# Kernel optimization log

Hardware: AMD Instinct MI355X
Metric: run time of the kernel (lower is better)

Reference implementation:

```python
import jax, jax.numpy as jnp
import numpy as np

B, T, E, H = 4, 1024, 1024, 16
F = E // H  # head_feature = 64
EPS = 1e-5


def setup_inputs() -> dict:
    key = jax.random.key(0)
    ks = jax.random.split(key, 7)
    return {
        "x": jax.random.normal(ks[0], (B, T, E), dtype=jnp.float32),
        "q_w": jax.random.normal(ks[1], (H, E, F), dtype=jnp.float32),
        "k_w": jax.random.normal(ks[2], (H, E, F), dtype=jnp.float32),
        "v_w": jax.random.normal(ks[3], (H, E, F), dtype=jnp.float32),
        "fr_w": jax.random.normal(ks[4], (B, E, E), dtype=jnp.float32),
        "ff_w": jax.random.normal(ks[5], (E, E), dtype=jnp.float32),
        "ff_b": jax.random.normal(ks[6], (E,), dtype=jnp.float32),
        "ln1_w": jnp.ones((T, E), dtype=jnp.float32),
        "ln1_b": jnp.zeros((T, E), dtype=jnp.float32),
        "ln2_w": jnp.ones((T, E), dtype=jnp.float32),
        "ln2_b": jnp.zeros((T, E), dtype=jnp.float32),
    }


def _layernorm_2d(x, w, b):
    # LayerNorm over the last TWO dims ([T, E]), matching nn.LayerNorm([T, E])
    mean = jnp.mean(x, axis=(-2, -1), keepdims=True)
    var = jnp.mean(jnp.square(x - mean), axis=(-2, -1), keepdims=True)
    return (x - mean) * jax.lax.rsqrt(var + EPS) * w + b


def _attention(x, q_w, k_w, v_w, fr_w):
    # projections: [B,T,E] x [H,E,F] -> [B,H,T,F]
    q = jnp.einsum("bte,hef->bhtf", x, q_w)
    k = jnp.einsum("bte,hef->bhtf", x, k_w)
    v = jnp.einsum("bte,hef->bhtf", x, v_w)
    scores = jnp.einsum("bhqf,bhkf->bhqk", q, k)  # [B,H,T,T]
    # faithful to source: multiplicative mask (-1e9 on strict upper tri, +1 added everywhere)
    ones = jnp.ones((T, T), dtype=scores.dtype)
    mask = -1.0e9 * jnp.triu(ones, k=1) + ones
    scores = scores * mask
    attn = jax.nn.softmax(scores / jnp.sqrt(jnp.float32(F)), axis=-1)
    z = jnp.einsum("bhqk,bhkf->bhqf", attn, v)  # [B,H,T,F]
    z = z.transpose(0, 2, 1, 3).reshape(B, T, E)  # merge heads
    return jnp.einsum("bte,bed->btd", z, fr_w)  # per-batch feature reduction


def reference(x, q_w, k_w, v_w, fr_w, ff_w, ff_b, ln1_w, ln1_b, ln2_w, ln2_b):
    z = _attention(x, q_w, k_w, v_w, fr_w)
    z1 = _layernorm_2d(x + z, ln1_w, ln1_b)
    z2 = jax.nn.relu(jnp.einsum("bte,de->btd", z1, ff_w) + ff_b)
    return _layernorm_2d(z1 + z2, ln2_w, ln2_b)
```

## Files before the change

### kernel.cpp

```cpp
#include <hip/hip_runtime.h>
#include <math.h>

constexpr int Bc = 4, Tc = 1024, Ec = 1024, Hc = 16, Fc = 64;

typedef __attribute__((ext_vector_type(8))) short bf16x8;
typedef __attribute__((ext_vector_type(4))) float f32x4;

__device__ __forceinline__ ushort f2bf(float x) {
  union { float f; unsigned u; } v; v.f = x;
  unsigned r = v.u + 0x7fffu + ((v.u >> 16) & 1u);
  return (ushort)(r >> 16);
}
__device__ __forceinline__ float bf2f(ushort h) {
  union { float f; unsigned u; } v; v.u = ((unsigned)h) << 16; return v.f;
}
__device__ __forceinline__ void split3(float x, ushort& h, ushort& m, ushort& l) {
  h = f2bf(x);
  float r1 = x - bf2f(h);
  m = f2bf(r1);
  float r2 = r1 - bf2f(m);
  l = f2bf(r2);
}
__device__ __forceinline__ void split2(float x, ushort& h, ushort& l) {
  h = f2bf(x);
  l = f2bf(x - bf2f(h));
}
__device__ __forceinline__ void split3t(float x, ushort& h, ushort& m, ushort& l) {
  union { float f; unsigned u; } v; v.f = x;
  h = (ushort)(v.u >> 16);
  union { float f; unsigned u; } hf; hf.u = v.u & 0xffff0000u;
  float r1 = x - hf.f;
  union { float f; unsigned u; } v1; v1.f = r1;
  m = (ushort)(v1.u >> 16);
  union { float f; unsigned u; } mf; mf.u = v1.u & 0xffff0000u;
  float r2 = r1 - mf.f;
  union { float f; unsigned u; } v2; v2.f = r2;
  l = (ushort)(v2.u >> 16);
}

#define FRAG_IDX(tile, quad, l) (((((tile) * 4) + (quad)) * 16 + (l)) * 8)

__global__ __launch_bounds__(256) void transp_w(
    const float* __restrict__ qw, const float* __restrict__ kw,
    const float* __restrict__ vw, ushort* __restrict__ wT)
{
  const int zi = blockIdx.z;
  const float* src = (zi == 0) ? qw : (zi == 1) ? kw : vw;
  ushort* dst = wT + (size_t)(zi * 3) * (1u << 20);
  const int ns = (zi == 2) ? 1 : 3;
  const int h = blockIdx.y, e0 = blockIdx.x * 64;
  __shared__ float T[64][68];
  const int tid = threadIdx.x;
  {
    const int er = tid >> 4, fr = (tid & 15) * 4;
#pragma unroll
    for (int i = 0; i < 4; ++i) {
      const float4 v = *(const float4*)&src[((size_t)(h * 1024 + e0 + er + i * 16)) * 64 + fr];
      *(float4*)&T[er + i * 16][fr] = v;
    }
  }
  __syncthreads();
  const int f = tid >> 2, eo = (tid & 3) * 16;
  ushort hs[16], ms[16], ls[16];
#pragma unroll
  for (int j = 0; j < 16; ++j) split3(T[eo + j][f], hs[j], ms[j], ls[j]);
  const size_t nbase = (size_t)(h * 64 + f) * 1024 + e0 + eo;
  bf16x8 v0, v1;
#pragma unroll
  for (int j = 0; j < 8; ++j) { v0[j] = (short)hs[j]; v1[j] = (short)hs[j + 8]; }
  *(bf16x8*)&dst[nbase] = v0; *(bf16x8*)&dst[nbase + 8] = v1;
  if (ns == 3) {
#pragma unroll
    for (int j = 0; j < 8; ++j) { v0[j] = (short)ms[j]; v1[j] = (short)ms[j + 8]; }
    *(bf16x8*)&dst[(1u << 20) + nbase] = v0; *(bf16x8*)&dst[(1u << 20) + nbase + 8] = v1;
#pragma unroll
    for (int j = 0; j < 8; ++j) { v0[j] = (short)ls[j]; v1[j] = (short)ls[j + 8]; }
    *(bf16x8*)&dst[(2u << 20) + nbase] = v0; *(bf16x8*)&dst[(2u << 20) + nbase + 8] = v1;
  }
}

__global__ __launch_bounds__(256) void transp_frw(
    const float* __restrict__ frw, ushort* __restrict__ frT)
{
  const int bb = blockIdx.z;
  const int e0 = blockIdx.x * 64, d0 = blockIdx.y * 64;
  __shared__ float T[64][68];
  const int tid = threadIdx.x;
  {
    const int er = tid >> 4, dr = (tid & 15) * 4;
#pragma unroll
    for (int i = 0; i < 4; ++i) {
      const float4 v = *(const float4*)&frw[((size_t)bb * 1024 + e0 + er + i * 16) * 1024 + d0 + dr];
      *(float4*)&T[er + i * 16][dr] = v;
    }
  }
  __syncthreads();
  const int d = tid >> 2, eo = (tid & 3) * 16;
  ushort hs[16], ls[16];
#pragma unroll
  for (int j = 0; j < 16; ++j) split2(T[eo + j][d], hs[j], ls[j]);
  const size_t nbase = ((size_t)bb * 1024 + d0 + d) * 1024 + e0 + eo;
  bf16x8 v0, v1;
#pragma unroll
  for (int j = 0; j < 8; ++j) { v0[j] = (short)hs[j]; v1[j] = (short)hs[j + 8]; }
  *(bf16x8*)&frT[nbase] = v0; *(bf16x8*)&frT[nbase + 8] = v1;
#pragma unroll
  for (int j = 0; j < 8; ++j) { v0[j] = (short)ls[j]; v1[j] = (short)ls[j + 8]; }
  *(bf16x8*)&frT[(4u << 20) + nbase] = v0; *(bf16x8*)&frT[(4u << 20) + nbase + 8] = v1;
}

__global__ __launch_bounds__(256) void proj_all_mfma(
    const float* __restrict__ x, const ushort* __restrict__ wT,
    float* __restrict__ qf, ushort* __restrict__ kh,
    ushort* __restrict__ km, ushort* __restrict__ kl,
    ushort* __restrict__ vt)
{
  const int zi = blockIdx.z;
  const int m0 = blockIdx.x * 128, n0 = blockIdx.y * 128;
  __shared__ ushort As[3 * 4096];
  __shared__ ushort Bs[3 * 4096];
  const int tid = threadIdx.x;
  const int wave = tid >> 6, lane = tid & 63, l15 = lane & 15, quad = lane >> 4;
  const int wm = wave >> 1, wn = wave & 1;
  const int sr = tid >> 1, q0 = (tid & 1) * 2;
  const int wb0 = FRAG_IDX(sr >> 4, q0, sr & 15);
  const int wb1 = FRAG_IDX(sr >> 4, q0 + 1, sr & 15);
  f32x4 acc[4][4] = {};

  if (zi < 2) {
    const ushort* wt = wT + (size_t)zi * 3 * (1u << 20);
    for (int k0 = 0; k0 < 1024; k0 += 32) {
      __syncthreads();
      {
        const float* ap = x + (size_t)(m0 + sr) * 1024 + k0 + q0 * 8;
        float xs[16];
        *(float4*)&xs[0]  = *(const float4*)(ap);
        *(float4*)&xs[4]  = *(const float4*)(ap + 4);
        *(float4*)&xs[8]  = *(const float4*)(ap + 8);
        *(float4*)&xs[12] = *(const float4*)(ap + 12);
        bf16x8 h0, h1, m0v, m1v, l0, l1;
#pragma unroll
        for (int j = 0; j < 8; ++j) {
          ushort hu, mu, lu;
          split3t(xs[j], hu, mu, lu);
          h0[j] = (short)hu; m0v[j] = (short)mu; l0[j] = (short)lu;
          split3t(xs[j + 8], hu, mu, lu);
          h1[j] = (short)hu; m1v[j] = (short)mu; l1[j] = (short)lu;
        }
        *(bf16x8*)&As[wb0] = h0;          *(bf16x8*)&As[wb1] = h1;
        *(bf16x8*)&As[4096 + wb0] = m0v;  *(bf16x8*)&As[4096 + wb1] = m1v;
        *(bf16x8*)&As[8192 + wb0] = l0;   *(bf16x8*)&As[8192 + wb1] = l1;
#pragma unroll
        for (int s = 0; s < 3; ++s) {
          const ushort* bp = wt + ((size_t)s << 20) + (size_t)(n0 + sr) * 1024 + k0 + q0 * 8;
          *(bf16x8*)&Bs[s * 4096 + wb0] = *(const bf16x8*)(bp);
          *(bf16x8*)&Bs[s * 4096 + wb1] = *(const bf16x8*)(bp + 8);
        }
      }
      __syncthreads();
      bf16x8 af[4][3];
#pragma unroll
      for (int tm = 0; tm < 4; ++tm)
#pragma unroll
        for (int s = 0; s < 3; ++s)
          af[tm][s] = *(const bf16x8*)&As[s * 4096 + FRAG_IDX(wm * 4 + tm, quad, l15)];
#pragma unroll
      for (int tn = 0; tn < 4; ++tn) {
        const int bi = FRAG_IDX(wn * 4 + tn, quad, l15);
        bf16x8 b0 = *(const bf16x8*)&Bs[bi];
        bf16x8 b1 = *(const bf16x8*)&Bs[4096 + bi];
        bf16x8 b2 = *(const bf16x8*)&Bs[8192 + bi];
#pragma unroll
        for (int tm = 0; tm < 4; ++tm) {
          f32x4 a = acc[tm][tn];
          a = __builtin_amdgcn_mfma_f32_16x16x32_bf16(af[tm][0], b0, a, 0, 0, 0);
          a = __builtin_amdgcn_mfma_f32_16x16x32_bf16(af[tm][0], b1, a, 0, 0, 0);
          a = __builtin_amdgcn_mfma_f32_16x16x32_bf16(af[tm][1], b0, a, 0, 0, 0);
          a = __builtin_amdgcn_mfma_f32_16x16x32_bf16(af[tm][0], b2, a, 0, 0, 0);
          a = __builtin_amdgcn_mfma_f32_16x16x32_bf16(af[tm][1], b1, a, 0, 0, 0);
          a = __builtin_amdgcn_mfma_f32_16x16x32_bf16(af[tm][2], b0, a, 0, 0, 0);
          acc[tm][tn] = a;
        }
      }
    }
#pragma unroll
    for (int tm = 0; tm < 4; ++tm) {
#pragma unroll
      for (int tn = 0; tn < 4; ++tn) {
#pragma unroll
        for (int r = 0; r < 4; ++r) {
          int m = m0 + wm * 64 + tm * 16 + quad * 4 + r;
          int n = n0 + wn * 64 + tn * 16 + l15;
          int b = m >> 10, t = m & 1023, h = n >> 6, f = n & 63;
          size_t idx = (((size_t)(b * 16 + h)) * 1024 + t) * 64 + f;
          if (zi == 0) {
            qf[idx] = acc[tm][tn][r];
          } else {
            ushort hu, mu, lu;
            split3(acc[tm][tn][r], hu, mu, lu);
            kh[idx] = hu; km[idx] = mu; kl[idx] = lu;
          }
        }
      }
    }
  } else {
    const ushort* wt = wT + (size_t)6 * (1u << 20);
    for (int k0 = 0; k0 < 1024; k0 += 32) {
      __syncthreads();
      {
        const float* ap = x + (size_t)(m0 + sr) * 1024 + k0 + q0 * 8;
        float xs[16];
        *(float4*)&xs[0]  = *(const float4*)(ap);
        *(float4*)&xs[4]  = *(const float4*)(ap + 4);
        *(float4*)&xs[8]  = *(const float4*)(ap + 8);
        *(float4*)&xs[12] = *(const float4*)(ap + 12);
        bf16x8 h0, h1;
#pragma unroll
        for (int j = 0; j < 8; ++j) {
          h0[j] = (short)f2bf(xs[j]);
          h1[j] = (short)f2bf(xs[j + 8]);
        }
        *(bf16x8*)&As[wb0] = h0; *(bf16x8*)&As[wb1] = h1;
        const ushort* bp = wt + (size_t)(n0 + sr) * 1024 + k0 + q0 * 8;
        *(bf16x8*)&Bs[wb0] = *(const bf16x8*)(bp);
        *(bf16x8*)&Bs[wb1] = *(const bf16x8*)(bp + 8);
      }
      __syncthreads();
      bf16x8 af[4];
#pragma unroll
      for (int tm = 0; tm < 4; ++tm)
        af[tm] = *(const bf16x8*)&As[FRAG_IDX(wm * 4 + tm, quad, l15)];
#pragma unroll
      for (int tn = 0; tn < 4; ++tn) {
        bf16x8 b0 = *(const bf16x8*)&Bs[FRAG_IDX(wn * 4 + tn, quad, l15)];
#pragma unroll
        for (int tm = 0; tm < 4; ++tm)
          acc[tm][tn] = __builtin_amdgcn_mfma_f32_16x16x32_bf16(af[tm], b0, acc[tm][tn], 0, 0, 0);
      }
    }
#pragma unroll
    for (int tm = 0; tm < 4; ++tm) {
#pragma unroll
      for (int tn = 0; tn < 4; ++tn) {
#pragma unroll
        for (int r = 0; r < 4; ++r) {
          int m = m0 + wm * 64 + tm * 16 + quad * 4 + r;
          int n = n0 + wn * 64 + tn * 16 + l15;
          int b = m >> 10, t = m & 1023, h = n >> 6, f = n & 63;
          vt[(((size_t)(b * 16 + h)) * 64 + f) * 1024 + t] = f2bf(acc[tm][tn][r]);
        }
      }
    }
  }
}

__global__ __launch_bounds__(512) void attn_mfma(
    const float* __restrict__ qf, const ushort* __restrict__ kh,
    const ushort* __restrict__ km, const ushort* __restrict__ kl,
    const ushort* __restrict__ vt, ushort* __restrict__ zh, ushort* __restrict__ zl)
{
  __shared__ ushort Ks[3][64][68];
  __shared__ ushort Vs[64][68];
  __shared__ ushort Pl[8][16][68];

  const int tid = threadIdx.x;
  const int wave = tid >> 6, lane = tid & 63;
  const int l15 = lane & 15, quad = lane >> 4;
  const int bh = blockIdx.y;
  const int qbase = blockIdx.x * 128;

  bf16x8 aqh[2], aqm[2], aql[2];
  {
    const int qrow = qbase + wave * 16 + l15;
    const float* qp = qf + ((size_t)bh * Tc + qrow) * Fc;
#pragma unroll
    for (int ks = 0; ks < 2; ++ks) {
      int f0 = ks * 32 + quad * 8;
      float4 x0 = *(const float4*)(qp + f0);
      float4 x1 = *(const float4*)(qp + f0 + 4);
      float xs[8] = {x0.x, x0.y, x0.z, x0.w, x1.x, x1.y, x1.z, x1.w};
#pragma unroll
      for (int j = 0; j < 8; ++j) {
        ushort hu, mu, lu;
        split3(xs[j], hu, mu, lu);
        aqh[ks][j] = (short)hu; aqm[ks][j] = (short)mu; aql[ks][j] = (short)lu;
      }
    }
  }

  f32x4 o[4] = {{0,0,0,0},{0,0,0,0},{0,0,0,0},{0,0,0,0}};
  float m_run[4], l_run[4];
#pragma unroll
  for (int r = 0; r < 4; ++r) { m_run[r] = -1e30f; l_run[r] = 0.f; }

  const int srow = tid >> 3, sc8 = tid & 7;
  const size_t kbase = (size_t)bh * Tc * Fc;
  const size_t vbase = (size_t)bh * Fc * Tc;
  const ushort* kp0 = kh + kbase + (size_t)srow * Fc + sc8 * 8;
  const ushort* kp1 = km + kbase + (size_t)srow * Fc + sc8 * 8;
  const ushort* kp2 = kl + kbase + (size_t)srow * Fc + sc8 * 8;
  const ushort* vp  = vt + vbase + (size_t)srow * Tc + sc8 * 8;

  for (int kt = 0; kt < Tc; kt += 64) {
    __syncthreads();
    {
      const size_t ko = (size_t)kt * Fc;
      *(bf16x8*)&Ks[0][srow][sc8 * 8] = *(const bf16x8*)(kp0 + ko);
      *(bf16x8*)&Ks[1][srow][sc8 * 8] = *(const bf16x8*)(kp1 + ko);
      *(bf16x8*)&Ks[2][srow][sc8 * 8] = *(const bf16x8*)(kp2 + ko);
      *(bf16x8*)&Vs[srow][sc8 * 8]    = *(const bf16x8*)(vp + kt);
    }
    __syncthreads();

    f32x4 sacc[4] = {{0,0,0,0},{0,0,0,0},{0,0,0,0},{0,0,0,0}};
#pragma unroll
    for (int nt = 0; nt < 4; ++nt) {
      int key = nt * 16 + l15;
#pragma unroll
      for (int ks = 0; ks < 2; ++ks) {
        int f0 = ks * 32 + quad * 8;
        bf16x8 bh_ = *(const bf16x8*)&Ks[0][key][f0];
        bf16x8 bm_ = *(const bf16x8*)&Ks[1][key][f0];
        bf16x8 bl_ = *(const bf16x8*)&Ks[2][key][f0];
        sacc[nt] = __builtin_amdgcn_mfma_f32_16x16x32_bf16(aqh[ks], bh_, sacc[nt], 0, 0, 0);
        sacc[nt] = __builtin_amdgcn_mfma_f32_16x16x32_bf16(aqh[ks], bm_, sacc[nt], 0, 0, 0);
        sacc[nt] = __builtin_amdgcn_mfma_f32_16x16x32_bf16(aqm[ks], bh_, sacc[nt], 0, 0, 0);
        sacc[nt] = __builtin_amdgcn_mfma_f32_16x16x32_bf16(aqh[ks], bl_, sacc[nt], 0, 0, 0);
        sacc[nt] = __builtin_amdgcn_mfma_f32_16x16x32_bf16(aqm[ks], bm_, sacc[nt], 0, 0, 0);
        sacc[nt] = __builtin_amdgcn_mfma_f32_16x16x32_bf16(aql[ks], bh_, sacc[nt], 0, 0, 0);
      }
    }

    const int rowg0 = qbase + wave * 16 + quad * 4;
    float mx[4];
#pragma unroll
    for (int r = 0; r < 4; ++r) mx[r] = -1e30f;
#pragma unroll
    for (int nt = 0; nt < 4; ++nt) {
      int key = kt + nt * 16 + l15;
#pragma unroll
      for (int r = 0; r < 4; ++r) {
        float s = sacc[nt][r];
        if (key > rowg0 + r) s *= -1.0e9f + 1.0f;
        s *= 0.125f;
        sacc[nt][r] = s;
        mx[r] = fmaxf(mx[r], s);
      }
    }
#pragma unroll
    for (int r = 0; r < 4; ++r)
#pragma unroll
      for (int d = 1; d < 16; d <<= 1) mx[r] = fmaxf(mx[r], __shfl_xor(mx[r], d));

    float corr[4], ps[4];
#pragma unroll
    for (int r = 0; r < 4; ++r) {
      float m2 = fmaxf(m_run[r], mx[r]);
      corr[r] = __expf(m_run[r] - m2);
      m_run[r] = m2;
      ps[r] = 0.f;
    }
#pragma unroll
    for (int nt = 0; nt < 4; ++nt) {
#pragma unroll
      for (int r = 0; r < 4; ++r) {
        float p = __expf(sacc[nt][r] - m_run[r]);
        ps[r] += p;
        Pl[wave][quad * 4 + r][nt * 16 + l15] = f2bf(p);
      }
    }
#pragma unroll
    for (int r = 0; r < 4; ++r) {
#pragma unroll
      for (int d = 1; d < 16; d <<= 1) ps[r] += __shfl_xor(ps[r], d);
      l_run[r] = l_run[r] * corr[r] + ps[r];
#pragma unroll
      for (int ft = 0; ft < 4; ++ft) o[ft][r] *= corr[r];
    }

#pragma unroll
    for (int ks2 = 0; ks2 < 2; ++ks2) {
      bf16x8 pa = *(const bf16x8*)&Pl[wave][l15][ks2 * 32 + quad * 8];
#pragma unroll
      for (int ft = 0; ft < 4; ++ft) {
        bf16x8 vb = *(const bf16x8*)&Vs[ft * 16 + l15][ks2 * 32 + quad * 8];
        o[ft] = __builtin_amdgcn_mfma_f32_16x16x32_bf16(pa, vb, o[ft], 0, 0, 0);
      }
    }
  }

  const int b = bh >> 4, h = bh & 15;
#pragma unroll
  for (int r = 0; r < 4; ++r) {
    float inv = 1.f / l_run[r];
    int row = qbase + wave * 16 + quad * 4 + r;
    size_t base = ((size_t)(b * Tc + row)) * Ec + h * Fc;
#pragma unroll
    for (int ft = 0; ft < 4; ++ft) {
      ushort hu, lu;
      split2(o[ft][r] * inv, hu, lu);
      zh[base + ft * 16 + l15] = hu;
      zl[base + ft * 16 + l15] = lu;
    }
  }
}

__global__ __launch_bounds__(256) void gemm_fr_mfma(
    const ushort* __restrict__ zh, const ushort* __restrict__ zl,
    const ushort* __restrict__ frT, const float* __restrict__ x,
    float* __restrict__ s1, float2* __restrict__ part)
{
  const int bb = blockIdx.z;
  const int m0 = blockIdx.x * 128, n0 = blockIdx.y * 64;
  __shared__ ushort Ah[4096], Al[4096], Bh[2048], Bl[2048];
  __shared__ float2 red[256];
  const int tid = threadIdx.x;
  const int wave = tid >> 6, lane = tid & 63, l15 = lane & 15, quad = lane >> 4;
  const int wm = wave >> 1, wn = wave & 1;
  const int sr = tid >> 1, q0 = (tid & 1) * 2;
  const int wb0 = FRAG_IDX(sr >> 4, q0, sr & 15);
  const int wb1 = FRAG_IDX(sr >> 4, q0 + 1, sr & 15);
  const int sr2 = tid >> 2, qb = tid & 3;
  const int wbB = FRAG_IDX(sr2 >> 4, qb, sr2 & 15);
  f32x4 acc[4][2] = {};
  const size_t abase = ((size_t)bb * 1024 + m0 + sr) * 1024 + q0 * 8;
  const size_t bbase = ((size_t)bb * 1024 + n0 + sr2) * 1024 + qb * 8;
  const ushort* blp = frT + (4u << 20);
  for (int k0 = 0; k0 < 1024; k0 += 32) {
    __syncthreads();
    {
      *(bf16x8*)&Ah[wb0] = *(const bf16x8*)(zh + abase + k0);
      *(bf16x8*)&Ah[wb1] = *(const bf16x8*)(zh + abase + k0 + 8);
      *(bf16x8*)&Al[wb0] = *(const bf16x8*)(zl + abase + k0);
      *(bf16x8*)&Al[wb1] = *(const bf16x8*)(zl + abase + k0 + 8);
      *(bf16x8*)&Bh[wbB] = *(const bf16x8*)(frT + bbase + k0);
      *(bf16x8*)&Bl[wbB] = *(const bf16x8*)(blp + bbase + k0);
    }
    __syncthreads();
    bf16x8 ah[4], al[4];
#pragma unroll
    for (int tm = 0; tm < 4; ++tm) {
      ah[tm] = *(const bf16x8*)&Ah[FRAG_IDX(wm * 4 + tm, quad, l15)];
      al[tm] = *(const bf16x8*)&Al[FRAG_IDX(wm * 4 + tm, quad, l15)];
    }
#pragma unroll
    for (int tn = 0; tn < 2; ++tn) {
      const int bi = FRAG_IDX(wn * 2 + tn, quad, l15);
      bf16x8 b0 = *(const bf16x8*)&Bh[bi];
      bf16x8 b1 = *(const bf16x8*)&Bl[bi];
#pragma unroll
      for (int tm = 0; tm < 4; ++tm) {
        f32x4 a = acc[tm][tn];
        a = __builtin_amdgcn_mfma_f32_16x16x32_bf16(ah[tm], b0, a, 0, 0, 0);
        a = __builtin_amdgcn_mfma_f32_16x16x32_bf16(ah[tm], b1, a, 0, 0, 0);
        a = __builtin_amdgcn_mfma_f32_16x16x32_bf16(al[tm], b0, a, 0, 0, 0);
        acc[tm][tn] = a;
      }
    }
  }
  float sum = 0.f, sq = 0.f;
#pragma unroll
  for (int tm = 0; tm < 4; ++tm) {
#pragma unroll
    for (int tn = 0; tn < 2; ++tn) {
#pragma unroll
      for (int r = 0; r < 4; ++r) {
        int m = m0 + wm * 64 + tm * 16 + quad * 4 + r;
        int n = n0 + wn * 32 + tn * 16 + l15;
        size_t idx = ((size_t)bb * 1024 + m) * 1024 + n;
        float o = x[idx] + acc[tm][tn][r];
        s1[idx] = o;
        sum += o; sq += o * o;
      }
    }
  }
  red[tid] = make_float2(sum, sq);
  __syncthreads();
  for (int s = 128; s > 0; s >>= 1) {
    if (tid < s) { red[tid].x += red[tid + s].x; red[tid].y += red[tid + s].y; }
    __syncthreads();
  }
  if (tid == 0) part[bb * 128 + blockIdx.x * 16 + blockIdx.y] = red[0];
}

__global__ __launch_bounds__(256) void gemm_ff_mfma(
    const ushort* __restrict__ z1h, const ushort* __restrict__ z1l,
    const ushort* __restrict__ fwh, const ushort* __restrict__ fwl,
    const float* __restrict__ ffb, float* __restrict__ s2,
    float2* __restrict__ part)
{
  const int m0 = blockIdx.x * 128, n0 = blockIdx.y * 64;
  __shared__ ushort Ah[4096], Al[4096], Bh[2048], Bl[2048];
  __shared__ float2 red[256];
  const int tid = threadIdx.x;
  const int wave = tid >> 6, lane = tid & 63, l15 = lane & 15, quad = lane >> 4;
  const int wm = wave >> 1, wn = wave & 1;
  const int sr = tid >> 1, q0 = (tid & 1) * 2;
  const int wb0 = FRAG_IDX(sr >> 4, q0, sr & 15);
  const int wb1 = FRAG_IDX(sr >> 4, q0 + 1, sr & 15);
  const int sr2 = tid >> 2, qb = tid & 3;
  const int wbB = FRAG_IDX(sr2 >> 4, qb, sr2 & 15);
  f32x4 acc[4][2] = {};
  const size_t abase = (size_t)(m0 + sr) * 1024 + q0 * 8;
  const size_t bbase = (size_t)(n0 + sr2) * 1024 + qb * 8;
  for (int k0 = 0; k0 < 1024; k0 += 32) {
    __syncthreads();
    {
      *(bf16x8*)&Ah[wb0] = *(const bf16x8*)(z1h + abase + k0);
      *(bf16x8*)&Ah[wb1] = *(const bf16x8*)(z1h + abase + k0 + 8);
      *(bf16x8*)&Al[wb0] = *(const bf16x8*)(z1l + abase + k0);
      *(bf16x8*)&Al[wb1] = *(const bf16x8*)(z1l + abase + k0 + 8);
      *(bf16x8*)&Bh[wbB] = *(const bf16x8*)(fwh + bbase + k0);
      *(bf16x8*)&Bl[wbB] = *(const bf16x8*)(fwl + bbase + k0);
    }
    __syncthreads();
    bf16x8 ah[4], al[4];
#pragma unroll
    for (int tm = 0; tm < 4; ++tm) {
      ah[tm] = *(const bf16x8*)&Ah[FRAG_IDX(wm * 4 + tm, quad, l15)];
      al[tm] = *(const bf16x8*)&Al[FRAG_IDX(wm * 4 + tm, quad, l15)];
    }
#pragma unroll
    for (int tn = 0; tn < 2; ++tn) {
      const int bi = FRAG_IDX(wn * 2 + tn, quad, l15);
      bf16x8 b0 = *(const bf16x8*)&Bh[bi];
      bf16x8 b1 = *(const bf16x8*)&Bl[bi];
#pragma unroll
      for (int tm = 0; tm < 4; ++tm) {
        f32x4 a = acc[tm][tn];
        a = __builtin_amdgcn_mfma_f32_16x16x32_bf16(ah[tm], b0, a, 0, 0, 0);
        a = __builtin_amdgcn_mfma_f32_16x16x32_bf16(ah[tm], b1, a, 0, 0, 0);
        a = __builtin_amdgcn_mfma_f32_16x16x32_bf16(al[tm], b0, a, 0, 0, 0);
        acc[tm][tn] = a;
      }
    }
  }
  float sum = 0.f, sq = 0.f;
#pragma unroll
  for (int tm = 0; tm < 4; ++tm) {
#pragma unroll
    for (int tn = 0; tn < 2; ++tn) {
#pragma unroll
      for (int r = 0; r < 4; ++r) {
        int m = m0 + wm * 64 + tm * 16 + quad * 4 + r;
        int n = n0 + wn * 32 + tn * 16 + l15;
        size_t idx = (size_t)m * 1024 + n;
        float z1v = bf2f(z1h[idx]) + bf2f(z1l[idx]);
        float o = z1v + fmaxf(acc[tm][tn][r] + ffb[n], 0.f);
        s2[idx] = o;
        sum += o; sq += o * o;
      }
    }
  }
  red[tid] = make_float2(sum, sq);
  __syncthreads();
  for (int s = 128; s > 0; s >>= 1) {
    if (tid < s) { red[tid].x += red[tid + s].x; red[tid].y += red[tid + s].y; }
    __syncthreads();
  }
  if (tid == 0) part[blockIdx.x * 16 + blockIdx.y] = red[0];
}

__global__ __launch_bounds__(256) void ln_stats(
    const float2* __restrict__ part, float2* __restrict__ stats, int npart)
{
  __shared__ double sd[256], sq[256];
  const int tid = threadIdx.x;
  double as = 0.0, aq = 0.0;
  for (int i = tid; i < npart; i += 256) {
    float2 p = part[blockIdx.x * npart + i];
    as += (double)p.x; aq += (double)p.y;
  }
  sd[tid] = as; sq[tid] = aq;
  __syncthreads();
  for (int s = 128; s > 0; s >>= 1) {
    if (tid < s) { sd[tid] += sd[tid + s]; sq[tid] += sq[tid + s]; }
    __syncthreads();
  }
  if (tid == 0) {
    const double n = (double)Tc * Ec;
    double mean = sd[0] / n;
    double var = sq[0] / n - mean * mean;
    if (var < 0.0) var = 0.0;
    double rs = 1.0 / sqrt(var + 1e-5);
    stats[blockIdx.x] = make_float2((float)mean, (float)rs);
  }
}

__global__ __launch_bounds__(256) void ln_norm_split(
    const float* __restrict__ s, const float2* __restrict__ stats,
    const float* __restrict__ w, const float* __restrict__ bias,
    ushort* __restrict__ oh, ushort* __restrict__ ol,
    const float* __restrict__ ffw, ushort* __restrict__ fwh, ushort* __restrict__ fwl)
{
  if (blockIdx.x >= 4096) {
    int i = (blockIdx.x - 4096) * 256 + threadIdx.x;
#pragma unroll
    for (int j = 0; j < 4; ++j) {
      int idx = i * 4 + j;
      float4 v = ((const float4*)ffw)[idx];
      ushort4 h, l;
      split2(v.x, h.x, l.x); split2(v.y, h.y, l.y);
      split2(v.z, h.z, l.z); split2(v.w, h.w, l.w);
      ((ushort4*)fwh)[idx] = h; ((ushort4*)fwl)[idx] = l;
    }
    return;
  }
  int i = blockIdx.x * 256 + threadIdx.x;
  int b = i >> 18;
  int te4 = i & ((1 << 18) - 1);
  float2 st = stats[b];
  float4 sv = ((const float4*)s)[i];
  float4 wv = ((const float4*)w)[te4];
  float4 bv = ((const float4*)bias)[te4];
  float4 o;
  o.x = (sv.x - st.x) * st.y * wv.x + bv.x;
  o.y = (sv.y - st.x) * st.y * wv.y + bv.y;
  o.z = (sv.z - st.x) * st.y * wv.z + bv.z;
  o.w = (sv.w - st.x) * st.y * wv.w + bv.w;
  ushort4 h, l;
  split2(o.x, h.x, l.x); split2(o.y, h.y, l.y);
  split2(o.z, h.z, l.z); split2(o.w, h.w, l.w);
  ((ushort4*)oh)[i] = h; ((ushort4*)ol)[i] = l;
}

__global__ __launch_bounds__(256) void ln_norm(
    const float* __restrict__ s, const float2* __restrict__ stats,
    const float* __restrict__ w, const float* __restrict__ bias,
    float* __restrict__ out)
{
  int i = blockIdx.x * 256 + threadIdx.x;
  if (i >= (Bc * Tc * Ec) / 4) return;
  int b = i >> 18;
  int te4 = i & ((1 << 18) - 1);
  float2 st = stats[b];
  float4 sv = ((const float4*)s)[i];
  float4 wv = ((const float4*)w)[te4];
  float4 bv = ((const float4*)bias)[te4];
  float4 o;
  o.x = (sv.x - st.x) * st.y * wv.x + bv.x;
  o.y = (sv.y - st.x) * st.y * wv.y + bv.y;
  o.z = (sv.z - st.x) * st.y * wv.z + bv.z;
  o.w = (sv.w - st.x) * st.y * wv.w + bv.w;
  ((float4*)out)[i] = o;
}

extern "C" void kernel_launch(void* const* d_in, const int* in_sizes, int n_in,
                              void* d_out, int out_size, void* d_ws, size_t ws_size,
                              hipStream_t stream)
{
  const float* x    = (const float*)d_in[0];
  const float* qw   = (const float*)d_in[1];
  const float* kw   = (const float*)d_in[2];
  const float* vw   = (const float*)d_in[3];
  const float* frw  = (const float*)d_in[4];
  const float* ffw  = (const float*)d_in[5];
  const float* ffb  = (const float*)d_in[6];
  const float* ln1w = (const float*)d_in[7];
  const float* ln1b = (const float*)d_in[8];
  const float* ln2w = (const float*)d_in[9];
  const float* ln2b = (const float*)d_in[10];
  float* out = (float*)d_out;
  char* W = (char*)d_ws;

  const size_t MB = 1ull << 20;
  float*  qf  = (float*)(W);
  ushort* kh  = (ushort*)(W + 16 * MB);
  ushort* km  = (ushort*)(W + 24 * MB);
  ushort* kl  = (ushort*)(W + 32 * MB);
  ushort* vt  = (ushort*)(W + 40 * MB);
  ushort* wT  = (ushort*)(W + 48 * MB);
  ushort* zh  = (ushort*)(W + 48 * MB);
  ushort* zl  = (ushort*)(W + 56 * MB);
  ushort* frT = (ushort*)(W + 16 * MB);
  float*  s1  = (float*)(W);
  ushort* z1h = (ushort*)(W + 16 * MB);
  ushort* z1l = (ushort*)(W + 24 * MB);
  ushort* fwh = (ushort*)(W + 48 * MB);
  ushort* fwl = (ushort*)(W + 50 * MB);
  float*  s2  = (float*)(W + 32 * MB);
  float2* part1  = (float2*)(W + 64 * MB);
  float2* part2  = part1 + 1024;
  float2* stats1 = part2 + 1024;
  float2* stats2 = stats1 + 4;

  transp_w<<<dim3(16, 16, 3), 256, 0, stream>>>(qw, kw, vw, wT);
  proj_all_mfma<<<dim3(32, 8, 3), 256, 0, stream>>>(x, wT, qf, kh, km, kl, vt);
  attn_mfma<<<dim3(8, 64), 512, 0, stream>>>(qf, kh, km, kl, vt, zh, zl);
  transp_frw<<<dim3(16, 16, 4), 256, 0, stream>>>(frw, frT);
  gemm_fr_mfma<<<dim3(8, 16, 4), 256, 0, stream>>>(zh, zl, frT, x, s1, part1);
  ln_stats<<<dim3(4), 256, 0, stream>>>(part1, stats1, 128);
  ln_norm_split<<<dim3(4352), 256, 0, stream>>>(s1, stats1, ln1w, ln1b, z1h, z1l,
                                                ffw, fwh, fwl);
  gemm_ff_mfma<<<dim3(32, 16), 256, 0, stream>>>(z1h, z1l, fwh, fwl, ffb, s2, part2);
  ln_stats<<<dim3(4), 256, 0, stream>>>(part2, stats2, 128);
  ln_norm<<<dim3(4096), 256, 0, stream>>>(s2, stats2, ln2w, ln2b, out);
}
```

Before: 420.8 us.

## Pre-tile projection weights and load them directly into LDS with register-prefetched x

The weight-transpose kernel now writes Q/K/V weights in a fragment-tiled layout, so each 32-wide k-slab of a 128-column tile is contiguous. The projection kernel can then stream B tiles straight into LDS with global_load_lds, skipping the trip through registers. It also prefetches the next x slab into registers a step ahead of use. The other GEMMs get per-lane staging indices that match the fragment layout, for more contiguous global and LDS access. This adds layout coupling between kernels and relies on the direct-to-LDS builtin placing data the way the fragment reads expect.

```diff
diff --git a/kernel.cpp b/kernel.cpp
--- a/kernel.cpp
+++ b/kernel.cpp
@@ -40,6 +40,12 @@
 
 #define FRAG_IDX(tile, quad, l) (((((tile) * 4) + (quad)) * 16 + (l)) * 8)
 
+__device__ __forceinline__ void gl_lds16(const ushort* g, ushort* s) {
+  __builtin_amdgcn_global_load_lds(
+      (__attribute__((address_space(1))) void*)(g),
+      (__attribute__((address_space(3))) void*)(s), 16, 0, 0);
+}
+
 __global__ __launch_bounds__(256) void transp_w(
     const float* __restrict__ qw, const float* __restrict__ kw,
     const float* __restrict__ vw, ushort* __restrict__ wT)
@@ -64,18 +70,23 @@
   ushort hs[16], ms[16], ls[16];
 #pragma unroll
   for (int j = 0; j < 16; ++j) split3(T[eo + j][f], hs[j], ms[j], ls[j]);
-  const size_t nbase = (size_t)(h * 64 + f) * 1024 + e0 + eo;
+  const int ntile = h >> 1;
+  const int ctile = ((h & 1) << 2) + (f >> 4);
+  const int kwx = (e0 + eo) >> 5;
+  const int qd = (eo & 16) >> 3;
+  const int c0 = ctile * 64 + qd * 16 + (f & 15);
+  const size_t nbase = ((size_t)(ntile * 32 + kwx)) * 4096 + (size_t)c0 * 8;
   bf16x8 v0, v1;
 #pragma unroll
   for (int j = 0; j < 8; ++j) { v0[j] = (short)hs[j]; v1[j] = (short)hs[j + 8]; }
-  *(bf16x8*)&dst[nbase] = v0; *(bf16x8*)&dst[nbase + 8] = v1;
+  *(bf16x8*)&dst[nbase] = v0; *(bf16x8*)&dst[nbase + 128] = v1;
   if (ns == 3) {
 #pragma unroll
     for (int j = 0; j < 8; ++j) { v0[j] = (short)ms[j]; v1[j] = (short)ms[j + 8]; }
-    *(bf16x8*)&dst[(1u << 20) + nbase] = v0; *(bf16x8*)&dst[(1u << 20) + nbase + 8] = v1;
+    *(bf16x8*)&dst[(1u << 20) + nbase] = v0; *(bf16x8*)&dst[(1u << 20) + nbase + 128] = v1;
 #pragma unroll
     for (int j = 0; j < 8; ++j) { v0[j] = (short)ls[j]; v1[j] = (short)ls[j + 8]; }
-    *(bf16x8*)&dst[(2u << 20) + nbase] = v0; *(bf16x8*)&dst[(2u << 20) + nbase + 8] = v1;
+    *(bf16x8*)&dst[(2u << 20) + nbase] = v0; *(bf16x8*)&dst[(2u << 20) + nbase + 128] = v1;
   }
 }
 
@@ -122,22 +133,32 @@
   const int tid = threadIdx.x;
   const int wave = tid >> 6, lane = tid & 63, l15 = lane & 15, quad = lane >> 4;
   const int wm = wave >> 1, wn = wave & 1;
-  const int sr = tid >> 1, q0 = (tid & 1) * 2;
-  const int wb0 = FRAG_IDX(sr >> 4, q0, sr & 15);
-  const int wb1 = FRAG_IDX(sr >> 4, q0 + 1, sr & 15);
+  const int ac1 = (wave * 64 + lane) * 8, ac2 = ac1 + 2048;
+  const size_t wrow = (size_t)(wave * 64 + lane) * 8;
   f32x4 acc[4][4] = {};
 
+  const float* ap1 = x + (size_t)(m0 + wave * 16 + l15) * 1024 + quad * 8;
+  const float* ap2 = ap1 + (size_t)64 * 1024;
+
+  float4 xa0 = *(const float4*)(ap1);
+  float4 xa1 = *(const float4*)(ap1 + 4);
+  float4 xb0 = *(const float4*)(ap2);
+  float4 xb1 = *(const float4*)(ap2 + 4);
+
   if (zi < 2) {
-    const ushort* wt = wT + (size_t)zi * 3 * (1u << 20);
-    for (int k0 = 0; k0 < 1024; k0 += 32) {
+    const ushort* wt = wT + (size_t)(zi * 3) * (1u << 20);
+    for (int kw = 0; kw < 32; ++kw) {
       __syncthreads();
+      float4 na0 = xa0, na1 = xa1, nb0 = xb0, nb1 = xb1;
+      if (kw < 31) {
+        const float* p1 = ap1 + (kw + 1) * 32;
+        const float* p2 = ap2 + (kw + 1) * 32;
+        na0 = *(const float4*)p1; na1 = *(const float4*)(p1 + 4);
+        nb0 = *(const float4*)p2; nb1 = *(const float4*)(p2 + 4);
+      }
       {
-        const float* ap = x + (size_t)(m0 + sr) * 1024 + k0 + q0 * 8;
-        float xs[16];
-        *(float4*)&xs[0]  = *(const float4*)(ap);
-        *(float4*)&xs[4]  = *(const float4*)(ap + 4);
-        *(float4*)&xs[8]  = *(const float4*)(ap + 8);
-        *(float4*)&xs[12] = *(const float4*)(ap + 12);
+        float xs[16] = {xa0.x, xa0.y, xa0.z, xa0.w, xa1.x, xa1.y, xa1.z, xa1.w,
+                        xb0.x, xb0.y, xb0.z, xb0.w, xb1.x, xb1.y, xb1.z, xb1.w};
         bf16x8 h0, h1, m0v, m1v, l0, l1;
 #pragma unroll
         for (int j = 0; j < 8; ++j) {
@@ -147,14 +168,17 @@
           split3t(xs[j + 8], hu, mu, lu);
           h1[j] = (short)hu; m1v[j] = (short)mu; l1[j] = (short)lu;
         }
-        *(bf16x8*)&As[wb0] = h0;          *(bf16x8*)&As[wb1] = h1;
-        *(bf16x8*)&As[4096 + wb0] = m0v;  *(bf16x8*)&As[4096 + wb1] = m1v;
-        *(bf16x8*)&As[8192 + wb0] = l0;   *(bf16x8*)&As[8192 + wb1] = l1;
+        *(bf16x8*)&As[ac1] = h0;          *(bf16x8*)&As[ac2] = h1;
+        *(bf16x8*)&As[4096 + ac1] = m0v;  *(bf16x8*)&As[4096 + ac2] = m1v;
+        *(bf16x8*)&As[8192 + ac1] = l0;   *(bf16x8*)&As[8192 + ac2] = l1;
+      }
+      {
+        const size_t wb = (size_t)(blockIdx.y * 32 + kw) * 4096;
 #pragma unroll
         for (int s = 0; s < 3; ++s) {
-          const ushort* bp = wt + ((size_t)s << 20) + (size_t)(n0 + sr) * 1024 + k0 + q0 * 8;
-          *(bf16x8*)&Bs[s * 4096 + wb0] = *(const bf16x8*)(bp);
-          *(bf16x8*)&Bs[s * 4096 + wb1] = *(const bf16x8*)(bp + 8);
+          const ushort* bsrc = wt + ((size_t)s << 20) + wb + wrow;
+          gl_lds16(bsrc, &Bs[s * 4096 + wave * 512]);
+          gl_lds16(bsrc + 2048, &Bs[s * 4096 + 2048 + wave * 512]);
         }
       }
       __syncthreads();
@@ -182,6 +206,7 @@
           acc[tm][tn] = a;
         }
       }
+      xa0 = na0; xa1 = na1; xb0 = nb0; xb1 = nb1;
     }
 #pragma unroll
     for (int tm = 0; tm < 4; ++tm) {
@@ -205,25 +230,31 @@
     }
   } else {
     const ushort* wt = wT + (size_t)6 * (1u << 20);
-    for (int k0 = 0; k0 < 1024; k0 += 32) {
+    for (int kw = 0; kw < 32; ++kw) {
       __syncthreads();
+      float4 na0 = xa0, na1 = xa1, nb0 = xb0, nb1 = xb1;
+      if (kw < 31) {
+        const float* p1 = ap1 + (kw + 1) * 32;
+        const float* p2 = ap2 + (kw + 1) * 32;
+        na0 = *(const float4*)p1; na1 = *(const float4*)(p1 + 4);
+        nb0 = *(const float4*)p2; nb1 = *(const float4*)(p2 + 4);
+      }
       {
-        const float* ap = x + (size_t)(m0 + sr) * 1024 + k0 + q0 * 8;
-        float xs[16];
-        *(float4*)&xs[0]  = *(const float4*)(ap);
-        *(float4*)&xs[4]  = *(const float4*)(ap + 4);
-        *(float4*)&xs[8]  = *(const float4*)(ap + 8);
-        *(float4*)&xs[12] = *(const float4*)(ap + 12);
+        float xs[16] = {xa0.x, xa0.y, xa0.z, xa0.w, xa1.x, xa1.y, xa1.z, xa1.w,
+                        xb0.x, xb0.y, xb0.z, xb0.w, xb1.x, xb1.y, xb1.z, xb1.w};
         bf16x8 h0, h1;
 #pragma unroll
         for (int j = 0; j < 8; ++j) {
           h0[j] = (short)f2bf(xs[j]);
           h1[j] = (short)f2bf(xs[j + 8]);
         }
-        *(bf16x8*)&As[wb0] = h0; *(bf16x8*)&As[wb1] = h1;
-        const ushort* bp = wt + (size_t)(n0 + sr) * 1024 + k0 + q0 * 8;
-        *(bf16x8*)&Bs[wb0] = *(const bf16x8*)(bp);
-        *(bf16x8*)&Bs[wb1] = *(const bf16x8*)(bp + 8);
+        *(bf16x8*)&As[ac1] = h0; *(bf16x8*)&As[ac2] = h1;
+      }
+      {
+        const size_t wb = (size_t)(blockIdx.y * 32 + kw) * 4096;
+        const ushort* bsrc = wt + wb + wrow;
+        gl_lds16(bsrc, &Bs[wave * 512]);
+        gl_lds16(bsrc + 2048, &Bs[2048 + wave * 512]);
       }
       __syncthreads();
       bf16x8 af[4];
@@ -237,6 +268,7 @@
         for (int tm = 0; tm < 4; ++tm)
           acc[tm][tn] = __builtin_amdgcn_mfma_f32_16x16x32_bf16(af[tm], b0, acc[tm][tn], 0, 0, 0);
       }
+      xa0 = na0; xa1 = na1; xb0 = nb0; xb1 = nb1;
     }
 #pragma unroll
     for (int tm = 0; tm < 4; ++tm) {
@@ -417,24 +449,22 @@
   const int tid = threadIdx.x;
   const int wave = tid >> 6, lane = tid & 63, l15 = lane & 15, quad = lane >> 4;
   const int wm = wave >> 1, wn = wave & 1;
-  const int sr = tid >> 1, q0 = (tid & 1) * 2;
-  const int wb0 = FRAG_IDX(sr >> 4, q0, sr & 15);
-  const int wb1 = FRAG_IDX(sr >> 4, q0 + 1, sr & 15);
-  const int sr2 = tid >> 2, qb = tid & 3;
-  const int wbB = FRAG_IDX(sr2 >> 4, qb, sr2 & 15);
+  const int ac1 = (wave * 64 + lane) * 8, ac2 = ac1 + 2048;
+  const int bc = (wave * 64 + lane) * 8;
   f32x4 acc[4][2] = {};
-  const size_t abase = ((size_t)bb * 1024 + m0 + sr) * 1024 + q0 * 8;
-  const size_t bbase = ((size_t)bb * 1024 + n0 + sr2) * 1024 + qb * 8;
+  const size_t abase1 = ((size_t)bb * 1024 + m0 + wave * 16 + l15) * 1024 + quad * 8;
+  const size_t abase2 = abase1 + (size_t)64 * 1024;
+  const size_t bbase = ((size_t)bb * 1024 + n0 + wave * 16 + l15) * 1024 + quad * 8;
   const ushort* blp = frT + (4u << 20);
   for (int k0 = 0; k0 < 1024; k0 += 32) {
     __syncthreads();
     {
-      *(bf16x8*)&Ah[wb0] = *(const bf16x8*)(zh + abase + k0);
-      *(bf16x8*)&Ah[wb1] = *(const bf16x8*)(zh + abase + k0 + 8);
-      *(bf16x8*)&Al[wb0] = *(const bf16x8*)(zl + abase + k0);
-      *(bf16x8*)&Al[wb1] = *(const bf16x8*)(zl + abase + k0 + 8);
-      *(bf16x8*)&Bh[wbB] = *(const bf16x8*)(frT + bbase + k0);
-      *(bf16x8*)&Bl[wbB] = *(const bf16x8*)(blp + bbase + k0);
+      *(bf16x8*)&Ah[ac1] = *(const bf16x8*)(zh + abase1 + k0);
+      *(bf16x8*)&Ah[ac2] = *(const bf16x8*)(zh + abase2 + k0);
+      *(bf16x8*)&Al[ac1] = *(const bf16x8*)(zl + abase1 + k0);
+      *(bf16x8*)&Al[ac2] = *(const bf16x8*)(zl + abase2 + k0);
+      *(bf16x8*)&Bh[bc] = *(const bf16x8*)(frT + bbase + k0);
+      *(bf16x8*)&Bl[bc] = *(const bf16x8*)(blp + bbase + k0);
     }
     __syncthreads();
     bf16x8 ah[4], al[4];
@@ -495,23 +525,21 @@
   const int tid = threadIdx.x;
   const int wave = tid >> 6, lane = tid & 63, l15 = lane & 15, quad = lane >> 4;
   const int wm = wave >> 1, wn = wave & 1;
-  const int sr = tid >> 1, q0 = (tid & 1) * 2;
-  const int wb0 = FRAG_IDX(sr >> 4, q0, sr & 15);
-  const int wb1 = FRAG_IDX(sr >> 4, q0 + 1, sr & 15);
-  const int sr2 = tid >> 2, qb = tid & 3;
-  const int wbB = FRAG_IDX(sr2 >> 4, qb, sr2 & 15);
+  const int ac1 = (wave * 64 + lane) * 8, ac2 = ac1 + 2048;
+  const int bc = (wave * 64 + lane) * 8;
   f32x4 acc[4][2] = {};
-  const size_t abase = (size_t)(m0 + sr) * 1024 + q0 * 8;
-  const size_t bbase = (size_t)(n0 + sr2) * 1024 + qb * 8;
+  const size_t abase1 = (size_t)(m0 + wave * 16 + l15) * 1024 + quad * 8;
+  const size_t abase2 = abase1 + (size_t)64 * 1024;
+  const size_t bbase = (size_t)(n0 + wave * 16 + l15) * 1024 + quad * 8;
   for (int k0 = 0; k0 < 1024; k0 += 32) {
     __syncthreads();
     {
-      *(bf16x8*)&Ah[wb0] = *(const bf16x8*)(z1h + abase + k0);
-      *(bf16x8*)&Ah[wb1] = *(const bf16x8*)(z1h + abase + k0 + 8);
-      *(bf16x8*)&Al[wb0] = *(const bf16x8*)(z1l + abase + k0);
-      *(bf16x8*)&Al[wb1] = *(const bf16x8*)(z1l + abase + k0 + 8);
-      *(bf16x8*)&Bh[wbB] = *(const bf16x8*)(fwh + bbase + k0);
-      *(bf16x8*)&Bl[wbB] = *(const bf16x8*)(fwl + bbase + k0);
+      *(bf16x8*)&Ah[ac1] = *(const bf16x8*)(z1h + abase1 + k0);
+      *(bf16x8*)&Ah[ac2] = *(const bf16x8*)(z1h + abase2 + k0);
+      *(bf16x8*)&Al[ac1] = *(const bf16x8*)(z1l + abase1 + k0);
+      *(bf16x8*)&Al[ac2] = *(const bf16x8*)(z1l + abase2 + k0);
+      *(bf16x8*)&Bh[bc] = *(const bf16x8*)(fwh + bbase + k0);
+      *(bf16x8*)&Bl[bc] = *(const bf16x8*)(fwl + bbase + k0);
     }
     __syncthreads();
     bf16x8 ah[4], al[4];
```

Result: slower. 460.3 us (+9.4%).
